# Kernel tuning notes

Measured on AMD Instinct MI355X. Metric: run time of the kernel, lower is better.

## Reference

```python
import jax, jax.numpy as jnp
import numpy as np

NEG_SLOPE = 0.1
N, D = 8192, 256


def setup_inputs() -> dict:
    key = jax.random.key(0)
    ks = jax.random.split(key, 7)
    head = jax.random.normal(ks[0], (N, D), dtype=jnp.float32)
    dependent = jax.random.normal(ks[1], (N, D), dtype=jnp.float32)
    alpha = jax.random.uniform(ks[2], (N, N), dtype=jnp.float32)
    # parameters (torch.rand init -> uniform [0,1))
    agg_weight_head = jax.random.uniform(ks[3], (D, D), dtype=jnp.float32)
    agg_weight_dependent = jax.random.uniform(ks[4], (D, D), dtype=jnp.float32)
    comb_weight_head = jax.random.uniform(ks[5], (D, D), dtype=jnp.float32)
    comb_weight_dependent = jax.random.uniform(ks[6], (D, D), dtype=jnp.float32)
    return {
        "head": head, "dependent": dependent, "alpha": alpha,
        "agg_weight_head": agg_weight_head,
        "agg_weight_dependent": agg_weight_dependent,
        "comb_weight_head": comb_weight_head,
        "comb_weight_dependent": comb_weight_dependent,
    }


def reference(head, dependent, alpha, agg_weight_head, agg_weight_dependent,
              comb_weight_head, comb_weight_dependent):
    # Double loop over j != i is equivalent to dense matmuls with the
    # diagonal contribution subtracted:
    #   head_agg[i]  = sum_j alpha[j,i]*head[j] + alpha[i,j]*dependent[j]  (j != i)
    #   dep_agg[i]   = sum_j alpha[i,j]*head[j] + alpha[j,i]*dependent[j]  (j != i)
    diag = jnp.diagonal(alpha)[:, None]                      # [N,1]
    hd_sum = head + dependent                                # [N,D]
    head_agg = alpha.T @ head + alpha @ dependent - diag * hd_sum
    dep_agg = alpha @ head + alpha.T @ dependent - diag * hd_sum
    head_out = jax.nn.leaky_relu(head_agg @ agg_weight_head + head @ comb_weight_head,
                                 negative_slope=NEG_SLOPE)
    dep_out = jax.nn.leaky_relu(dep_agg @ agg_weight_dependent + dependent @ comb_weight_dependent,
                                negative_slope=NEG_SLOPE)
    return (head_out, dep_out)
```

## Files before the change

### kernel.cpp

```cpp
#include <hip/hip_runtime.h>

#define NN 8192
#define DD 256
#define ND_ (NN * DD)

#define NEG_SLOPE 0.1f

typedef _Float16 half8 __attribute__((ext_vector_type(8)));
typedef _Float16 half4 __attribute__((ext_vector_type(4)));
typedef float f32x4 __attribute__((ext_vector_type(4)));
typedef float f32x16 __attribute__((ext_vector_type(16)));

__device__ __forceinline__ void ld_g2l16(const void* g, void* l) {
    __builtin_amdgcn_global_load_lds(
        (const __attribute__((address_space(1))) void*)g,
        (__attribute__((address_space(3))) void*)l, 16, 0, 0);
}

__device__ __forceinline__ unsigned pkhalf2(_Float16 a, _Float16 b) {
    unsigned short ua = __builtin_bit_cast(unsigned short, a);
    unsigned short ub = __builtin_bit_cast(unsigned short, b);
    return (unsigned)ua | ((unsigned)ub << 16);
}

__global__ __launch_bounds__(256, 4)
void prep_split_kernel(const float* __restrict__ h, const float* __restrict__ d,
                       _Float16* __restrict__ uS_hi, _Float16* __restrict__ vS_hi) {
    __shared__ float s_h[64 * 68];
    __shared__ float s_d[64 * 68];
    const int b  = blockIdx.x;
    const int kt = b >> 2;
    const int ct = b & 3;
    const int k0 = kt * 64;
    const int c0 = ct * 64;
    const int t  = threadIdx.x;

#pragma unroll
    for (int e = 0; e < 4; ++e) {
        int idx = e * 256 + t;
        int r   = idx >> 4;
        int c4  = (idx & 15) << 2;
        float4 hv = *(const float4*)&h[(size_t)(k0 + r) * DD + c0 + c4];
        float4 dv = *(const float4*)&d[(size_t)(k0 + r) * DD + c0 + c4];
        *(float4*)&s_h[r * 68 + c4] = hv;
        *(float4*)&s_d[r * 68 + c4] = dv;
    }
    __syncthreads();

#pragma unroll
    for (int e = 0; e < 2; ++e) {
        int idx = e * 256 + t;
        int c   = idx >> 3;
        int seg = idx & 7;
        half8 uh, vh;
#pragma unroll
        for (int m = 0; m < 8; ++m) {
            float hh = s_h[(seg * 8 + m) * 68 + c];
            float dd = s_d[(seg * 8 + m) * 68 + c];
            uh[m] = (_Float16)(hh + dd);
            vh[m] = (_Float16)(hh - dd);
        }
        int    cg   = c0 + c;
        int    kb   = kt * 2 + (seg >> 2);
        int    slot = (seg & 3) ^ ((cg >> 1) & 3);
        size_t go   = (size_t)kb * 8192 + (size_t)cg * 32 + slot * 8;
        *(half8*)&uS_hi[go] = uh;
        *(half8*)&vS_hi[go] = vh;
    }
}

__global__ __launch_bounds__(512, 6)
void agg_mfma_kernel(const float* __restrict__ alpha,
                     const _Float16* __restrict__ uS_hi, const _Float16* __restrict__ vS_hi,
                     _Float16* __restrict__ Pbuf,
                     _Float16* __restrict__ Qbuf) {
    __shared__ __align__(16) unsigned char smem[53248];

    const int raw  = blockIdx.x;
    const int kh   = raw & 1;
    const int cb   = (raw >> 3) & 1;
    const int rb   = ((raw >> 1) & 3) | ((raw >> 4) << 2);
    const int I0   = rb * 64;
    const int C0   = cb * 128;
    const int t    = threadIdx.x;
    const int w    = t >> 6;
    const int lane = t & 63;

    const bool isP = (w < 4);
    const int  cw  = w & 3;

    f32x16 acc0, acc1;
#pragma unroll
    for (int r = 0; r < 16; ++r) { acc0[r] = 0.f; acc1[r] = 0.f; }

    const int rbase = t & 15;
    const int kp    = (t >> 4) & 15;
    const int dup   = t >> 8;
    const int rowa  = rbase + 32 * dup;
    const int lrow  = lane & 31;
    const int lk    = (lane >> 5) << 3;
    const int kbase = kh * (NN / 2);
    const int c_local = cw * 32 + lrow;

#define LOAD_ALPHA(S, IT)                                                        \
    {                                                                            \
        const int kk0 = kbase + (IT) * 32 + 2 * kp;                              \
        size_t z0 = (size_t)kk0 * NN + I0;                                       \
        S##c00 = alpha[z0 + rowa];                                               \
        S##c01 = alpha[z0 + NN + rowa];                                          \
        S##c10 = alpha[z0 + rowa + 16];                                          \
        S##c11 = alpha[z0 + NN + rowa + 16];                                     \
        S##r0  = *(const float2*)&alpha[(size_t)(I0 + rowa) * NN + kk0];         \
        S##r1  = *(const float2*)&alpha[(size_t)(I0 + rowa + 16) * NN + kk0];    \
    }

#define ITER(CUR, P, IT)                                                         \
    {                                                                            \
                   \
        unsigned su0 = pkhalf2((_Float16)(CUR##c00 + CUR##r0.x), (_Float16)(CUR##c01 + CUR##r0.y)); \
        unsigned du0 = pkhalf2((_Float16)(CUR##c00 - CUR##r0.x), (_Float16)(CUR##c01 - CUR##r0.y)); \
        unsigned su1 = pkhalf2((_Float16)(CUR##c10 + CUR##r1.x), (_Float16)(CUR##c11 + CUR##r1.y)); \
        unsigned du1 = pkhalf2((_Float16)(CUR##c10 - CUR##r1.x), (_Float16)(CUR##c11 - CUR##r1.y)); \
                          \
        {                                                                        \
            unsigned* wS = (unsigned*)(smem + (P) * 10240);                      \
            unsigned* wD = (unsigned*)(smem + (P) * 10240 + 5120);               \
            wS[rowa * 20 + kp]        = su0;                                     \
            wS[(rowa + 16) * 20 + kp] = su1;                                     \
            wD[rowa * 20 + kp]        = du0;                                     \
            wD[(rowa + 16) * 20 + kp] = du1;                                     \
        }                                                                        \
               \
        asm volatile("s_waitcnt vmcnt(6)" ::: "memory");                         \
        asm volatile("s_waitcnt lgkmcnt(0)" ::: "memory");                       \
        __builtin_amdgcn_s_barrier();                                            \
        __builtin_amdgcn_sched_barrier(0);                                       \
           \
        {                                                                        \
            size_t gb = (size_t)(kh * 128 + (((IT) + 1) & 127)) * 8192 +         \
                        cb * 4096 + (size_t)(w * 512 + lane * 8);                \
            unsigned char* bN = smem + 20480 + (1 - (P)) * 16384;                \
            ld_g2l16(uS_hi + gb, bN + w * 1024);                                 \
            ld_g2l16(vS_hi + gb, bN + 8192 + w * 1024);                          \
        }                                                                        \
        __builtin_amdgcn_sched_barrier(0);         \
                 \
        LOAD_ALPHA(CUR, (((IT) + 2) & 127))                                      \
        __builtin_amdgcn_sched_barrier(0);                                       \
                                    \
        {                                                                        \
            const unsigned char* sd = smem + (P) * 10240;                        \
            const _Float16* aSD = (const _Float16*)(sd + (isP ? 0 : 5120));      \
            const unsigned char* bb = smem + 20480 + (P) * 16384;                \
            const _Float16* bB  = (const _Float16*)(bb + (isP ? 0 : 8192));      \
            __builtin_amdgcn_s_setprio(1);                                       \
            _Pragma("unroll")                                                    \
            for (int s = 0; s < 2; ++s) {                                        \
                int gd = s * 2 + (lane >> 5);                                    \
                int sl = gd ^ ((c_local >> 1) & 3);                              \
                int bi = c_local * 32 + sl * 8;                                  \
                half8 aH0 = *(const half8*)&aSD[(lrow) * 40 + s * 16 + lk];      \
                half8 aH1 = *(const half8*)&aSD[(32 + lrow) * 40 + s * 16 + lk]; \
                half8 bH  = *(const half8*)&bB[bi];                              \
                acc0 = __builtin_amdgcn_mfma_f32_32x32x16_f16(aH0, bH, acc0, 0, 0, 0); \
                acc1 = __builtin_amdgcn_mfma_f32_32x32x16_f16(aH1, bH, acc1, 0, 0, 0); \
            }                                                                    \
            __builtin_amdgcn_s_setprio(0);                                       \
        }                                                                        \
    }

    float Ac00, Ac01, Ac10, Ac11;
    float2 Ar0, Ar1;
    float Bc00, Bc01, Bc10, Bc11;
    float2 Br0, Br1;

    LOAD_ALPHA(A, 0)
    LOAD_ALPHA(B, 1)
    {
        size_t gb = (size_t)(kh * 128) * 8192 + cb * 4096 +
                    (size_t)(w * 512 + lane * 8);
        unsigned char* bN = smem + 20480;
        ld_g2l16(uS_hi + gb, bN + w * 1024);
        ld_g2l16(vS_hi + gb, bN + 8192 + w * 1024);
    }

    for (int it2 = 0; it2 < 64; ++it2) {
        ITER(A, 0, (it2 * 2))
        ITER(B, 1, (it2 * 2 + 1))
    }
#undef ITER
#undef LOAD_ALPHA

    _Float16* dst = (isP ? Pbuf : Qbuf) + (size_t)kh * ND_;
    const int colw = C0 + cw * 32 + (lane & 31);
#pragma unroll
    for (int reg = 0; reg < 16; ++reg) {
        int rr = (reg & 3) + ((reg >> 2) << 3) + ((lane >> 5) << 2);
        dst[(size_t)(I0 + rr) * DD + colw]      = (_Float16)acc0[reg];
        dst[(size_t)(I0 + 32 + rr) * DD + colw] = (_Float16)acc1[reg];
    }
}

__global__ __launch_bounds__(256, 4)
void stageB_kernel(const _Float16* __restrict__ Pbuf, const _Float16* __restrict__ Qbuf,
                   const float* __restrict__ head, const float* __restrict__ dep,
                   const float* __restrict__ alpha,
                   const float* __restrict__ Wah, const float* __restrict__ Wad,
                   const float* __restrict__ Wch, const float* __restrict__ Wcd,
                   float* __restrict__ out) {
    __shared__ float smem2[12544];
    __shared__ float s_dg[64];
    float* s_x  = smem2;
    float* s_y  = smem2 + 2176;
    float* s_w1 = smem2 + 4352;
    float* s_w2 = smem2 + 8448;

    int b   = blockIdx.x;
    int sel = b >> 8;
    int rem = b & 255;
    int rb  = rem >> 1;
    int cb  = rem & 1;
    int I0  = rb * 64;
    int C0  = cb * 128;

    const float* Y  = sel ? dep : head;
    const float* W1 = sel ? Wad : Wah;
    const float* W2 = sel ? Wcd : Wch;
    float* dst = out + sel * ND_;

    int t  = threadIdx.x;
    int rg = t & 15, cg = t >> 4;
    int r0 = rg * 4, c0 = cg * 8;

    if (t < 64) s_dg[t] = alpha[(size_t)(I0 + t) * NN + I0 + t];

    float acc[4][8];
#pragma unroll
    for (int i = 0; i < 4; ++i)
#pragma unroll
        for (int j = 0; j < 8; ++j) acc[i][j] = 0.0f;

    for (int it = 0; it < 8; ++it) {
        int k0 = it * 32;
        __syncthreads();
#pragma unroll
        for (int e = 0; e < 2; ++e) {
            int idx = e * 256 + t;
            int r   = idx >> 3;
            int k4  = (idx & 7) << 2;
            size_t go = (size_t)(I0 + r) * DD + k0 + k4;
            half4 p0 = *(const half4*)&Pbuf[go];
            half4 p1 = *(const half4*)&Pbuf[ND_ + go];
            half4 q0 = *(const half4*)&Qbuf[go];
            half4 q1 = *(const half4*)&Qbuf[ND_ + go];
            float4 hv = *(const float4*)&head[go];
            float4 dv = *(const float4*)&dep[go];
            float dgv = s_dg[r];
            float hj[4] = {hv.x, hv.y, hv.z, hv.w};
            float dj[4] = {dv.x, dv.y, dv.z, dv.w};
#pragma unroll
            for (int j = 0; j < 4; ++j) {
                float Pv = (float)p0[j] + (float)p1[j];
                float Qv = (float)q0[j] + (float)q1[j];
                float uu = hj[j] + dj[j];
                float x  = (sel ? 0.5f * (Pv - Qv) : 0.5f * (Pv + Qv)) - dgv * uu;
                s_x[(k4 + j) * 68 + r] = x;
                s_y[(k4 + j) * 68 + r] = sel ? dj[j] : hj[j];
            }
        }
#pragma unroll
        for (int e = 0; e < 4; ++e) {
            int idx = e * 256 + t;
            int kkk = idx >> 5;
            int c4  = (idx & 31) << 2;
            *(float4*)&s_w1[kkk * 128 + c4] =
                *(const float4*)&W1[(size_t)(k0 + kkk) * DD + C0 + c4];
            *(float4*)&s_w2[kkk * 128 + c4] =
                *(const float4*)&W2[(size_t)(k0 + kkk) * DD + C0 + c4];
        }
        __syncthreads();
#pragma unroll 8
        for (int k = 0; k < 32; ++k) {
            float4 xv = *(const float4*)&s_x[k * 68 + r0];
            float4 yv = *(const float4*)&s_y[k * 68 + r0];
            float4 wa = *(const float4*)&s_w1[k * 128 + c0];
            float4 wb = *(const float4*)&s_w1[k * 128 + c0 + 4];
            float4 wc = *(const float4*)&s_w2[k * 128 + c0];
            float4 wd = *(const float4*)&s_w2[k * 128 + c0 + 4];
            float xs[4]  = {xv.x, xv.y, xv.z, xv.w};
            float ys[4]  = {yv.x, yv.y, yv.z, yv.w};
            float w1s[8] = {wa.x, wa.y, wa.z, wa.w, wb.x, wb.y, wb.z, wb.w};
            float w2s[8] = {wc.x, wc.y, wc.z, wc.w, wd.x, wd.y, wd.z, wd.w};
#pragma unroll
            for (int i = 0; i < 4; ++i)
#pragma unroll
                for (int j = 0; j < 8; ++j)
                    acc[i][j] += xs[i] * w1s[j] + ys[i] * w2s[j];
        }
    }

#pragma unroll
    for (int i = 0; i < 4; ++i) {
#pragma unroll
        for (int jv = 0; jv < 2; ++jv) {
            float4 o;
            float v0 = acc[i][4 * jv + 0];
            float v1 = acc[i][4 * jv + 1];
            float v2 = acc[i][4 * jv + 2];
            float v3 = acc[i][4 * jv + 3];
            o.x = v0 >= 0.0f ? v0 : NEG_SLOPE * v0;
            o.y = v1 >= 0.0f ? v1 : NEG_SLOPE * v1;
            o.z = v2 >= 0.0f ? v2 : NEG_SLOPE * v2;
            o.w = v3 >= 0.0f ? v3 : NEG_SLOPE * v3;
            *(float4*)&dst[(size_t)(I0 + r0 + i) * DD + C0 + c0 + 4 * jv] = o;
        }
    }
}

extern "C" void kernel_launch(void* const* d_in, const int* in_sizes, int n_in,
                              void* d_out, int out_size, void* d_ws, size_t ws_size,
                              hipStream_t stream) {
    const float* head  = (const float*)d_in[0];
    const float* dep   = (const float*)d_in[1];
    const float* alpha = (const float*)d_in[2];
    const float* Wah   = (const float*)d_in[3];
    const float* Wad   = (const float*)d_in[4];
    const float* Wch   = (const float*)d_in[5];
    const float* Wcd   = (const float*)d_in[6];
    float* out = (float*)d_out;

    _Float16* ws    = (_Float16*)d_ws;
    _Float16* uS_hi = ws;
    _Float16* vS_hi = ws + (size_t)ND_;
    _Float16* Pbuf  = ws + (size_t)2 * ND_;
    _Float16* Qbuf  = ws + (size_t)4 * ND_;

    prep_split_kernel<<<512, 256, 0, stream>>>(head, dep, uS_hi, vS_hi);
    agg_mfma_kernel<<<512, 512, 0, stream>>>(alpha, uS_hi, vS_hi, Pbuf, Qbuf);
    stageB_kernel<<<512, 256, 0, stream>>>(Pbuf, Qbuf, head, dep, alpha,
                                           Wah, Wad, Wch, Wcd, out);
}
```

Before: 285.5 us.

## Halve agg kernel block to 256 threads with 64x64 per-wave MFMA tiles

Shrinks the aggregation kernel from 8 to 4 waves per block while keeping the same block tile. Each wave now computes a 64x64 output tile (four 32x32 accumulators) instead of 64x32, and each thread loads and converts twice as much alpha and B data per iteration. The goal is to reuse each A fragment across two B fragments, which cuts LDS reads per MFMA and the per-thread sync overhead. In exchange, register pressure rises and there are fewer waves to hide latency.

New measurement: 290.8 us. Within noise of the previous version (+1.8%).

```diff
diff --git a/kernel.cpp b/kernel.cpp
--- a/kernel.cpp
+++ b/kernel.cpp
@@ -69,7 +69,7 @@
     }
 }
 
-__global__ __launch_bounds__(512, 6)
+__global__ __launch_bounds__(256, 3)
 void agg_mfma_kernel(const float* __restrict__ alpha,
                      const _Float16* __restrict__ uS_hi, const _Float16* __restrict__ vS_hi,
                      _Float16* __restrict__ Pbuf,
@@ -86,68 +86,79 @@
     const int w    = t >> 6;
     const int lane = t & 63;
 
-    const bool isP = (w < 4);
-    const int  cw  = w & 3;
-
-    f32x16 acc0, acc1;
-#pragma unroll
-    for (int r = 0; r < 16; ++r) { acc0[r] = 0.f; acc1[r] = 0.f; }
+    const bool isP = (w < 2);
+    const int  cw  = w & 1;
+
+    f32x16 acc00, acc01, acc10, acc11;
+#pragma unroll
+    for (int r = 0; r < 16; ++r) {
+        acc00[r] = 0.f; acc01[r] = 0.f; acc10[r] = 0.f; acc11[r] = 0.f;
+    }
 
     const int rbase = t & 15;
     const int kp    = (t >> 4) & 15;
-    const int dup   = t >> 8;
-    const int rowa  = rbase + 32 * dup;
+    const int row0  = rbase;
+    const int row1  = rbase + 16;
+    const int row2  = rbase + 32;
+    const int row3  = rbase + 48;
     const int lrow  = lane & 31;
     const int lk    = (lane >> 5) << 3;
     const int kbase = kh * (NN / 2);
-    const int c_local = cw * 32 + lrow;
 
 #define LOAD_ALPHA(S, IT)                                                        \
     {                                                                            \
         const int kk0 = kbase + (IT) * 32 + 2 * kp;                              \
         size_t z0 = (size_t)kk0 * NN + I0;                                       \
-        S##c00 = alpha[z0 + rowa];                                               \
-        S##c01 = alpha[z0 + NN + rowa];                                          \
-        S##c10 = alpha[z0 + rowa + 16];                                          \
-        S##c11 = alpha[z0 + NN + rowa + 16];                                     \
-        S##r0  = *(const float2*)&alpha[(size_t)(I0 + rowa) * NN + kk0];         \
-        S##r1  = *(const float2*)&alpha[(size_t)(I0 + rowa + 16) * NN + kk0];    \
+        S##c00 = alpha[z0 + row0];      S##c10 = alpha[z0 + NN + row0];          \
+        S##c01 = alpha[z0 + row1];      S##c11 = alpha[z0 + NN + row1];          \
+        S##c02 = alpha[z0 + row2];      S##c12 = alpha[z0 + NN + row2];          \
+        S##c03 = alpha[z0 + row3];      S##c13 = alpha[z0 + NN + row3];          \
+        S##r0 = *(const float2*)&alpha[(size_t)(I0 + row0) * NN + kk0];          \
+        S##r1 = *(const float2*)&alpha[(size_t)(I0 + row1) * NN + kk0];          \
+        S##r2 = *(const float2*)&alpha[(size_t)(I0 + row2) * NN + kk0];          \
+        S##r3 = *(const float2*)&alpha[(size_t)(I0 + row3) * NN + kk0];          \
     }
 
 #define ITER(CUR, P, IT)                                                         \
     {                                                                            \
                    \
-        unsigned su0 = pkhalf2((_Float16)(CUR##c00 + CUR##r0.x), (_Float16)(CUR##c01 + CUR##r0.y)); \
-        unsigned du0 = pkhalf2((_Float16)(CUR##c00 - CUR##r0.x), (_Float16)(CUR##c01 - CUR##r0.y)); \
-        unsigned su1 = pkhalf2((_Float16)(CUR##c10 + CUR##r1.x), (_Float16)(CUR##c11 + CUR##r1.y)); \
-        unsigned du1 = pkhalf2((_Float16)(CUR##c10 - CUR##r1.x), (_Float16)(CUR##c11 - CUR##r1.y)); \
+        unsigned s0 = pkhalf2((_Float16)(CUR##c00 + CUR##r0.x), (_Float16)(CUR##c10 + CUR##r0.y)); \
+        unsigned d0 = pkhalf2((_Float16)(CUR##c00 - CUR##r0.x), (_Float16)(CUR##c10 - CUR##r0.y)); \
+        unsigned s1 = pkhalf2((_Float16)(CUR##c01 + CUR##r1.x), (_Float16)(CUR##c11 + CUR##r1.y)); \
+        unsigned d1 = pkhalf2((_Float16)(CUR##c01 - CUR##r1.x), (_Float16)(CUR##c11 - CUR##r1.y)); \
+        unsigned s2 = pkhalf2((_Float16)(CUR##c02 + CUR##r2.x), (_Float16)(CUR##c12 + CUR##r2.y)); \
+        unsigned d2 = pkhalf2((_Float16)(CUR##c02 - CUR##r2.x), (_Float16)(CUR##c12 - CUR##r2.y)); \
+        unsigned s3 = pkhalf2((_Float16)(CUR##c03 + CUR##r3.x), (_Float16)(CUR##c13 + CUR##r3.y)); \
+        unsigned d3 = pkhalf2((_Float16)(CUR##c03 - CUR##r3.x), (_Float16)(CUR##c13 - CUR##r3.y)); \
                           \
         {                                                                        \
             unsigned* wS = (unsigned*)(smem + (P) * 10240);                      \
             unsigned* wD = (unsigned*)(smem + (P) * 10240 + 5120);               \
-            wS[rowa * 20 + kp]        = su0;                                     \
-            wS[(rowa + 16) * 20 + kp] = su1;                                     \
-            wD[rowa * 20 + kp]        = du0;                                     \
-            wD[(rowa + 16) * 20 + kp] = du1;                                     \
+            wS[row0 * 20 + kp] = s0;  wD[row0 * 20 + kp] = d0;                   \
+            wS[row1 * 20 + kp] = s1;  wD[row1 * 20 + kp] = d1;                   \
+            wS[row2 * 20 + kp] = s2;  wD[row2 * 20 + kp] = d2;                   \
+            wS[row3 * 20 + kp] = s3;  wD[row3 * 20 + kp] = d3;                   \
         }                                                                        \
-               \
-        asm volatile("s_waitcnt vmcnt(6)" ::: "memory");                         \
+            \
+        asm volatile("s_waitcnt vmcnt(12)" ::: "memory");                        \
         asm volatile("s_waitcnt lgkmcnt(0)" ::: "memory");                       \
         __builtin_amdgcn_s_barrier();                                            \
         __builtin_amdgcn_sched_barrier(0);                                       \
            \
         {                                                                        \
             size_t gb = (size_t)(kh * 128 + (((IT) + 1) & 127)) * 8192 +         \
-                        cb * 4096 + (size_t)(w * 512 + lane * 8);                \
+                        cb * 4096 + (size_t)(w * 1024 + lane * 8);               \
             unsigned char* bN = smem + 20480 + (1 - (P)) * 16384;                \
-            ld_g2l16(uS_hi + gb, bN + w * 1024);                                 \
-            ld_g2l16(vS_hi + gb, bN + 8192 + w * 1024);                          \
+            ld_g2l16(uS_hi + gb,       bN + w * 2048);                           \
+            ld_g2l16(uS_hi + gb + 512, bN + w * 2048 + 1024);                    \
+            ld_g2l16(vS_hi + gb,       bN + 8192 + w * 2048);                    \
+            ld_g2l16(vS_hi + gb + 512, bN + 8192 + w * 2048 + 1024);             \
         }                                                                        \
         __builtin_amdgcn_sched_barrier(0);         \
                  \
         LOAD_ALPHA(CUR, (((IT) + 2) & 127))                                      \
         __builtin_amdgcn_sched_barrier(0);                                       \
-                                    \
+                   \
         {                                                                        \
             const unsigned char* sd = smem + (P) * 10240;                        \
             const _Float16* aSD = (const _Float16*)(sd + (isP ? 0 : 5120));      \
@@ -156,33 +167,40 @@
             __builtin_amdgcn_s_setprio(1);                                       \
             _Pragma("unroll")                                                    \
             for (int s = 0; s < 2; ++s) {                                        \
-                int gd = s * 2 + (lane >> 5);                                    \
-                int sl = gd ^ ((c_local >> 1) & 3);                              \
-                int bi = c_local * 32 + sl * 8;                                  \
                 half8 aH0 = *(const half8*)&aSD[(lrow) * 40 + s * 16 + lk];      \
                 half8 aH1 = *(const half8*)&aSD[(32 + lrow) * 40 + s * 16 + lk]; \
-                half8 bH  = *(const half8*)&bB[bi];                              \
-                acc0 = __builtin_amdgcn_mfma_f32_32x32x16_f16(aH0, bH, acc0, 0, 0, 0); \
-                acc1 = __builtin_amdgcn_mfma_f32_32x32x16_f16(aH1, bH, acc1, 0, 0, 0); \
+                int gd = s * 2 + (lane >> 5);                                    \
+                int c0l = cw * 64 + lrow;                                        \
+                int sl0 = gd ^ ((c0l >> 1) & 3);                                 \
+                half8 bH0 = *(const half8*)&bB[c0l * 32 + sl0 * 8];              \
+                int c1l = cw * 64 + 32 + lrow;                                   \
+                int sl1 = gd ^ ((c1l >> 1) & 3);                                 \
+                half8 bH1 = *(const half8*)&bB[c1l * 32 + sl1 * 8];              \
+                acc00 = __builtin_amdgcn_mfma_f32_32x32x16_f16(aH0, bH0, acc00, 0, 0, 0); \
+                acc10 = __builtin_amdgcn_mfma_f32_32x32x16_f16(aH1, bH0, acc10, 0, 0, 0); \
+                acc01 = __builtin_amdgcn_mfma_f32_32x32x16_f16(aH0, bH1, acc01, 0, 0, 0); \
+                acc11 = __builtin_amdgcn_mfma_f32_32x32x16_f16(aH1, bH1, acc11, 0, 0, 0); \
             }                                                                    \
             __builtin_amdgcn_s_setprio(0);                                       \
         }                                                                        \
     }
 
-    float Ac00, Ac01, Ac10, Ac11;
-    float2 Ar0, Ar1;
-    float Bc00, Bc01, Bc10, Bc11;
-    float2 Br0, Br1;
-
+    float Ac00, Ac10, Ac01, Ac11, Ac02, Ac12, Ac03, Ac13;
+    float2 Ar0, Ar1, Ar2, Ar3;
+    float Bc00, Bc10, Bc01, Bc11, Bc02, Bc12, Bc03, Bc13;
+    float2 Br0, Br1, Br2, Br3;
+
+    {
+        size_t gb = (size_t)(kh * 128) * 8192 + cb * 4096 +
+                    (size_t)(w * 1024 + lane * 8);
+        unsigned char* bN = smem + 20480;
+        ld_g2l16(uS_hi + gb,       bN + w * 2048);
+        ld_g2l16(uS_hi + gb + 512, bN + w * 2048 + 1024);
+        ld_g2l16(vS_hi + gb,       bN + 8192 + w * 2048);
+        ld_g2l16(vS_hi + gb + 512, bN + 8192 + w * 2048 + 1024);
+    }
     LOAD_ALPHA(A, 0)
     LOAD_ALPHA(B, 1)
-    {
-        size_t gb = (size_t)(kh * 128) * 8192 + cb * 4096 +
-                    (size_t)(w * 512 + lane * 8);
-        unsigned char* bN = smem + 20480;
-        ld_g2l16(uS_hi + gb, bN + w * 1024);
-        ld_g2l16(vS_hi + gb, bN + 8192 + w * 1024);
-    }
 
     for (int it2 = 0; it2 < 64; ++it2) {
         ITER(A, 0, (it2 * 2))
@@ -192,12 +210,14 @@
 #undef LOAD_ALPHA
 
     _Float16* dst = (isP ? Pbuf : Qbuf) + (size_t)kh * ND_;
-    const int colw = C0 + cw * 32 + (lane & 31);
+    const int colw0 = C0 + cw * 64 + (lane & 31);
 #pragma unroll
     for (int reg = 0; reg < 16; ++reg) {
         int rr = (reg & 3) + ((reg >> 2) << 3) + ((lane >> 5) << 2);
-        dst[(size_t)(I0 + rr) * DD + colw]      = (_Float16)acc0[reg];
-        dst[(size_t)(I0 + 32 + rr) * DD + colw] = (_Float16)acc1[reg];
+        dst[(size_t)(I0 + rr) * DD + colw0]           = (_Float16)acc00[reg];
+        dst[(size_t)(I0 + 32 + rr) * DD + colw0]      = (_Float16)acc10[reg];
+        dst[(size_t)(I0 + rr) * DD + colw0 + 32]      = (_Float16)acc01[reg];
+        dst[(size_t)(I0 + 32 + rr) * DD + colw0 + 32] = (_Float16)acc11[reg];
     }
 }
 
@@ -336,7 +356,7 @@
     _Float16* Qbuf  = ws + (size_t)4 * ND_;
 
     prep_split_kernel<<<512, 256, 0, stream>>>(head, dep, uS_hi, vS_hi);
-    agg_mfma_kernel<<<512, 512, 0, stream>>>(alpha, uS_hi, vS_hi, Pbuf, Qbuf);
+    agg_mfma_kernel<<<512, 256, 0, stream>>>(alpha, uS_hi, vS_hi, Pbuf, Qbuf);
     stageB_kernel<<<512, 256, 0, stream>>>(Pbuf, Qbuf, head, dep, alpha,
                                            Wah, Wad, Wch, Wcd, out);
 }
```
